# Kernel optimization log

Hardware: AMD Instinct MI355X
Metric: run time of the kernel (lower is better)

Reference implementation:

```python
import jax, jax.numpy as jnp
import numpy as np

NUM_NODES = 100000
NUM_EDGES = 1600000
DIM = 64
NUM_LAYERS = 3


def setup_inputs() -> dict:
    key = jax.random.key(0)
    k1, k2 = jax.random.split(key)
    x = jax.random.normal(k1, (NUM_NODES, DIM), dtype=jnp.float32)
    adj_t = jax.random.randint(k2, (2, NUM_EDGES), 0, NUM_NODES, dtype=jnp.int64)
    return {"x": x, "adj_t": adj_t}


def reference(x, adj_t):
    n = x.shape[0]
    # undirected -> add reversed edges (adj_t_is_undirected=True path)
    edge_index = jnp.concatenate([adj_t, adj_t[::-1]], axis=1)  # [2, 2E]
    row, col = edge_index[0], edge_index[1]
    edge_weight = jnp.ones((row.shape[0],), dtype=x.dtype)
    # gcn_norm: D^-0.5 A D^-0.5 (degree computed by scatter over col)
    deg = jax.ops.segment_sum(edge_weight, col, num_segments=n)
    deg_inv_sqrt = jnp.where(deg > 0, jax.lax.rsqrt(deg), 0.0).astype(x.dtype)
    w = deg_inv_sqrt[row] * edge_weight * deg_inv_sqrt[col]  # [2E]
    outs = [x]
    for _ in range(NUM_LAYERS):
        # gather -> scale -> scatter_add (SpMM)
        msgs = w[:, None] * x[row]                     # [2E, D]
        x = jax.ops.segment_sum(msgs, col, num_segments=n)  # [N, D]
        outs.append(x)
    return jnp.mean(jnp.stack(outs), axis=0)
```

## Files before the change

### kernel.cpp

```cpp
#include <hip/hip_runtime.h>

#define DIM 64
#define BKT_SHIFT 7
#define BKT_G 128
#define NBLK 256
#define HIST_B 1024
#define NREP 4
#define CAP 4608
#define RCAP 18

__device__ inline float blo(unsigned p) { return __uint_as_float(p << 16); }
__device__ inline float bhi(unsigned p) { return __uint_as_float(p & 0xffff0000u); }
__device__ inline unsigned bpack(float x, float y) {
    unsigned ux = __float_as_uint(x);
    unsigned uy = __float_as_uint(y);
    ux += 0x7fffu + ((ux >> 16) & 1u);
    uy += 0x7fffu + ((uy >> 16) & 1u);
    return (ux >> 16) | (uy & 0xffff0000u);
}

__global__ void zero_kernel(int* __restrict__ p, int n) {
    int i = blockIdx.x * blockDim.x + threadIdx.x;
    if (i < n) p[i] = 0;
}

__global__ __launch_bounds__(HIST_B)
void place_direct_kernel(const int* __restrict__ adj, int E,
                         int* __restrict__ gcnt,
                         unsigned* __restrict__ pairs, int NB) {
    extern __shared__ int lds[];
    int* lh  = lds;
    int* cur = lds + NREP * NB;
    for (int g = threadIdx.x; g < (NREP + 1) * NB; g += blockDim.x) lds[g] = 0;
    __syncthreads();
    const int rep = (threadIdx.x & (NREP - 1)) * NB;
    const int n4 = E >> 2;
    const int4* srcs = (const int4*)adj;
    const int4* dsts = (const int4*)(adj + E);

    int4 a0 = {0,0,0,0}, b0 = a0, a1 = a0, b1 = a0;
    int have = 0;
    for (int i = blockIdx.x * blockDim.x + threadIdx.x; i < n4;
         i += NBLK * blockDim.x) {
        int4 a = srcs[i];
        int4 b = dsts[i];
        atomicAdd(&lh[rep + (a.x >> BKT_SHIFT)], 1);
        atomicAdd(&lh[rep + (a.y >> BKT_SHIFT)], 1);
        atomicAdd(&lh[rep + (a.z >> BKT_SHIFT)], 1);
        atomicAdd(&lh[rep + (a.w >> BKT_SHIFT)], 1);
        atomicAdd(&lh[rep + (b.x >> BKT_SHIFT)], 1);
        atomicAdd(&lh[rep + (b.y >> BKT_SHIFT)], 1);
        atomicAdd(&lh[rep + (b.z >> BKT_SHIFT)], 1);
        atomicAdd(&lh[rep + (b.w >> BKT_SHIFT)], 1);
        if (have == 0)      { a0 = a; b0 = b; have = 1; }
        else if (have == 1) { a1 = a; b1 = b; have = 2; }
    }
    int te = 0, ta = 0, tb = 0;
    if (blockIdx.x == 0) {
        for (int e = (n4 << 2) + threadIdx.x; e < E; e += blockDim.x) {
            int a = adj[e];
            int b = adj[E + e];
            atomicAdd(&lh[rep + (a >> BKT_SHIFT)], 1);
            atomicAdd(&lh[rep + (b >> BKT_SHIFT)], 1);
            if (te == 0) { ta = a; tb = b; te = 1; }
        }
    }
    __syncthreads();
    for (int g = threadIdx.x; g < NB; g += blockDim.x) {
        int tot = lh[g] + lh[NB + g] + lh[2 * NB + g] + lh[3 * NB + g];
        cur[g] = (tot > 0) ? atomicAdd(&gcnt[g], tot) : 0;
    }
    __syncthreads();
#define PLACE_EMIT(av, bv)                                                     \
    {                                                                          \
        int gb = (bv) >> BKT_SHIFT;                                            \
        int p = atomicAdd(&cur[gb], 1);                                        \
        if (p < CAP)                                                           \
            pairs[(size_t)gb * CAP + p] =                                      \
                ((unsigned)((bv) & (BKT_G - 1)) << 17) | (unsigned)(av);       \
        int ga = (av) >> BKT_SHIFT;                                            \
        p = atomicAdd(&cur[ga], 1);                                            \
        if (p < CAP)                                                           \
            pairs[(size_t)ga * CAP + p] =                                      \
                ((unsigned)((av) & (BKT_G - 1)) << 17) | (unsigned)(bv);       \
    }
    if (have >= 1) {
        PLACE_EMIT(a0.x, b0.x); PLACE_EMIT(a0.y, b0.y);
        PLACE_EMIT(a0.z, b0.z); PLACE_EMIT(a0.w, b0.w);
    }
    if (have >= 2) {
        PLACE_EMIT(a1.x, b1.x); PLACE_EMIT(a1.y, b1.y);
        PLACE_EMIT(a1.z, b1.z); PLACE_EMIT(a1.w, b1.w);
    }
    {
        int it = 0;
        for (int i = blockIdx.x * blockDim.x + threadIdx.x; i < n4;
             i += NBLK * blockDim.x) {
            if (it >= 2) {
                int4 a = srcs[i];
                int4 b = dsts[i];
                PLACE_EMIT(a.x, b.x); PLACE_EMIT(a.y, b.y);
                PLACE_EMIT(a.z, b.z); PLACE_EMIT(a.w, b.w);
            }
            ++it;
        }
    }
    if (blockIdx.x == 0) {
        int tl = 0;
        for (int e = (n4 << 2) + threadIdx.x; e < E; e += blockDim.x) {
            if (tl == 0 && te == 1) {
                PLACE_EMIT(ta, tb);
            } else {
                int a = adj[e];
                int b = adj[E + e];
                PLACE_EMIT(a, b);
            }
            ++tl;
        }
    }
#undef PLACE_EMIT
}

__global__ void scan782_kernel(const int* __restrict__ gcnt,
                               int* __restrict__ bsums, int nb) {
    __shared__ int tmp[1024];
    int v = (threadIdx.x < nb) ? gcnt[threadIdx.x] : 0;
    tmp[threadIdx.x] = v;
    __syncthreads();
    for (int off = 1; off < 1024; off <<= 1) {
        int t = (threadIdx.x >= off) ? tmp[threadIdx.x - off] : 0;
        __syncthreads();
        tmp[threadIdx.x] += t;
        __syncthreads();
    }
    if (threadIdx.x < nb) bsums[threadIdx.x] = tmp[threadIdx.x] - v;
}

__global__ __launch_bounds__(256)
void pass2_build_kernel(const unsigned* __restrict__ pairs,
                        const int* __restrict__ gcnt,
                        const int* __restrict__ bsums,
                        const float4* __restrict__ x,
                        int* __restrict__ csr_src,
                        int* __restrict__ row_ptr,
                        int* __restrict__ deg,
                        float* __restrict__ dinv,
                        uint4* __restrict__ xs0,
                        int N, int NB, int total_adj) {
    __shared__ int cnt[BKT_G];
    __shared__ int pre[BKT_G];
    __shared__ int cur[BKT_G];
    __shared__ float dv[BKT_G];
    int g = blockIdx.x;
    int base = g << BKT_SHIFT;
    size_t poff = (size_t)g * CAP;
    int m = gcnt[g];
    if (m > CAP) m = CAP;
    int coff = bsums[g];
    if (threadIdx.x < BKT_G) cnt[threadIdx.x] = 0;
    __syncthreads();
    unsigned rec[RCAP];
#pragma unroll
    for (int k = 0; k < RCAP; ++k) {
        int i = threadIdx.x + k * 256;
        unsigned p = 0;
        if (i < m) {
            p = pairs[poff + i];
            atomicAdd(&cnt[p >> 17], 1);
        }
        rec[k] = p;
    }
    __syncthreads();
    if (threadIdx.x < BKT_G) pre[threadIdx.x] = cnt[threadIdx.x];
    __syncthreads();
    for (int o = 1; o < BKT_G; o <<= 1) {
        int t = 0;
        if (threadIdx.x < BKT_G && threadIdx.x >= o) t = pre[threadIdx.x - o];
        __syncthreads();
        if (threadIdx.x < BKT_G) pre[threadIdx.x] += t;
        __syncthreads();
    }
    if (threadIdx.x < BKT_G) {
        int v = base + threadIdx.x;
        if (v < N) {
            int c = cnt[threadIdx.x];
            int start = coff + pre[threadIdx.x] - c;
            float di = (c > 0) ? rsqrtf((float)c) : 0.0f;
            row_ptr[v] = start;
            deg[v] = c;
            dinv[v] = di;
            dv[threadIdx.x] = di;
            cur[threadIdx.x] = start;
        }
    }
    if (g == NB - 1 && threadIdx.x == 0) row_ptr[N] = total_adj;
    __syncthreads();
#pragma unroll
    for (int k = 0; k < RCAP; ++k) {
        int i = threadIdx.x + k * 256;
        if (i < m) {
            unsigned p = rec[k];
            int pos = atomicAdd(&cur[p >> 17], 1);
            csr_src[pos] = (int)(p & 0x1ffffu);
        }
    }
    for (int w = threadIdx.x; w < BKT_G * 8; w += blockDim.x) {
        int vl = w >> 3, sub = w & 7;
        int v = base + vl;
        if (v < N) {
            float di = dv[vl];
            float4 xa = x[(size_t)v * 16 + sub * 2];
            float4 xb = x[(size_t)v * 16 + sub * 2 + 1];
            uint4 o;
            o.x = bpack(di * xa.x, di * xa.y);
            o.y = bpack(di * xa.z, di * xa.w);
            o.z = bpack(di * xb.x, di * xb.y);
            o.w = bpack(di * xb.z, di * xb.w);
            xs0[(size_t)v * 8 + sub] = o;
        }
    }
}

#define SPMM_ACCUM_BODY                                                        \
    int half = threadIdx.x & 31;                                               \
    int nb = half >> 3, sub = half & 7;                                        \
    int beg = row_ptr[v];                                                      \
    int end = row_ptr[v + 1];                                                  \
    int full = (end - beg) >> 4;                                               \
    float a0 = 0, a1 = 0, a2 = 0, a3 = 0, a4 = 0, a5 = 0, a6 = 0, a7 = 0;      \
    int j = beg;                                                               \
    int s0 = 0, s1 = 0, s2 = 0, s3 = 0;                                        \
    if (full > 0) {                                                            \
        int b = j + 4 * nb;                                                    \
        s0 = csr_src[b];     s1 = csr_src[b + 1];                              \
        s2 = csr_src[b + 2]; s3 = csr_src[b + 3];                              \
    }                                                                          \
    for (int it = 0; it < full; ++it) {                                        \
        int jn = j + 16;                                                       \
        int t0 = 0, t1 = 0, t2 = 0, t3 = 0;                                    \
        if (it + 1 < full) {                                                   \
            int b = jn + 4 * nb;                                               \
            t0 = csr_src[b];     t1 = csr_src[b + 1];                          \
            t2 = csr_src[b + 2]; t3 = csr_src[b + 3];                          \
        }                                                                      \
        uint4 p0 = xs_in[(size_t)s0 * 8 + sub];                                \
        uint4 p1 = xs_in[(size_t)s1 * 8 + sub];                                \
        uint4 p2 = xs_in[(size_t)s2 * 8 + sub];                                \
        uint4 p3 = xs_in[(size_t)s3 * 8 + sub];                                \
        a0 += (blo(p0.x) + blo(p1.x)) + (blo(p2.x) + blo(p3.x));               \
        a1 += (bhi(p0.x) + bhi(p1.x)) + (bhi(p2.x) + bhi(p3.x));               \
        a2 += (blo(p0.y) + blo(p1.y)) + (blo(p2.y) + blo(p3.y));               \
        a3 += (bhi(p0.y) + bhi(p1.y)) + (bhi(p2.y) + bhi(p3.y));               \
        a4 += (blo(p0.z) + blo(p1.z)) + (blo(p2.z) + blo(p3.z));               \
        a5 += (bhi(p0.z) + bhi(p1.z)) + (bhi(p2.z) + bhi(p3.z));               \
        a6 += (blo(p0.w) + blo(p1.w)) + (blo(p2.w) + blo(p3.w));               \
        a7 += (bhi(p0.w) + bhi(p1.w)) + (bhi(p2.w) + bhi(p3.w));               \
        s0 = t0; s1 = t1; s2 = t2; s3 = t3;                                    \
        j = jn;                                                                \
    }                                                                          \
    for (int idx = j + nb; idx < end; idx += 4) {                              \
        int s = csr_src[idx];                                                  \
        uint4 p = xs_in[(size_t)s * 8 + sub];                                  \
        a0 += blo(p.x); a1 += bhi(p.x);                                        \
        a2 += blo(p.y); a3 += bhi(p.y);                                        \
        a4 += blo(p.z); a5 += bhi(p.z);                                        \
        a6 += blo(p.w); a7 += bhi(p.w);                                        \
    }                                                                          \
    a0 += __shfl_xor(a0, 8);  a0 += __shfl_xor(a0, 16);                        \
    a1 += __shfl_xor(a1, 8);  a1 += __shfl_xor(a1, 16);                        \
    a2 += __shfl_xor(a2, 8);  a2 += __shfl_xor(a2, 16);                        \
    a3 += __shfl_xor(a3, 8);  a3 += __shfl_xor(a3, 16);                        \
    a4 += __shfl_xor(a4, 8);  a4 += __shfl_xor(a4, 16);                        \
    a5 += __shfl_xor(a5, 8);  a5 += __shfl_xor(a5, 16);                        \
    a6 += __shfl_xor(a6, 8);  a6 += __shfl_xor(a6, 16);                        \
    a7 += __shfl_xor(a7, 8);  a7 += __shfl_xor(a7, 16);

__global__ void spmm_bf16_kernel(const int* __restrict__ row_ptr,
                                 const int* __restrict__ csr_src,
                                 const float* __restrict__ dinv,
                                 const uint4* __restrict__ xs_in,
                                 uint4* __restrict__ xs_out, int N) {
    int t = blockIdx.x * blockDim.x + threadIdx.x;
    int v = t >> 5;
    if (v >= N) return;
    SPMM_ACCUM_BODY
    if (nb == 0) {
        float di = dinv[v];
        float d2 = di * di;
        uint4 o;
        o.x = bpack(d2 * a0, d2 * a1);
        o.y = bpack(d2 * a2, d2 * a3);
        o.z = bpack(d2 * a4, d2 * a5);
        o.w = bpack(d2 * a6, d2 * a7);
        xs_out[(size_t)v * 8 + sub] = o;
    }
}

__global__ void spmm_last_kernel(const int* __restrict__ row_ptr,
                                 const int* __restrict__ csr_src,
                                 const float* __restrict__ dinv,
                                 const int* __restrict__ deg,
                                 const uint4* __restrict__ xs_in,
                                 const uint4* __restrict__ xs1,
                                 const float4* __restrict__ x,
                                 float4* __restrict__ out, int N) {
    int t = blockIdx.x * blockDim.x + threadIdx.x;
    int v = t >> 5;
    if (v >= N) return;
    SPMM_ACCUM_BODY
    if (nb == 0) {
        float di = dinv[v];
        float rs = sqrtf((float)deg[v]);
        size_t idx = (size_t)v * 8 + sub;
        uint4 q1 = xs1[idx];
        uint4 q2 = xs_in[idx];
        float4 xa = x[(size_t)v * 16 + sub * 2];
        float4 xb = x[(size_t)v * 16 + sub * 2 + 1];
        float4 oa, ob;
        oa.x = 0.25f * (xa.x + rs * (blo(q1.x) + blo(q2.x)) + di * a0);
        oa.y = 0.25f * (xa.y + rs * (bhi(q1.x) + bhi(q2.x)) + di * a1);
        oa.z = 0.25f * (xa.z + rs * (blo(q1.y) + blo(q2.y)) + di * a2);
        oa.w = 0.25f * (xa.w + rs * (bhi(q1.y) + bhi(q2.y)) + di * a3);
        ob.x = 0.25f * (xb.x + rs * (blo(q1.z) + blo(q2.z)) + di * a4);
        ob.y = 0.25f * (xb.y + rs * (bhi(q1.z) + bhi(q2.z)) + di * a5);
        ob.z = 0.25f * (xb.z + rs * (blo(q1.w) + blo(q2.w)) + di * a6);
        ob.w = 0.25f * (xb.w + rs * (bhi(q1.w) + bhi(q2.w)) + di * a7);
        out[(size_t)v * 16 + sub * 2]     = oa;
        out[(size_t)v * 16 + sub * 2 + 1] = ob;
    }
}

extern "C" void kernel_launch(void* const* d_in, const int* in_sizes, int n_in,
                              void* d_out, int out_size, void* d_ws, size_t ws_size,
                              hipStream_t stream) {
    const float* x = (const float*)d_in[0];
    const int* adj = (const int*)d_in[1];
    float* out     = (float*)d_out;

    const int total_adj = in_sizes[1];
    const int E = total_adj / 2;
    const int N = in_sizes[0] / DIM;
    const int NB = (N + BKT_G - 1) / BKT_G;

    size_t BUF = (size_t)total_adj * 4;
    size_t xsb = (size_t)N * 32 * 4;
    if (xsb > BUF) BUF = xsb;
    BUF = (BUF + 255) & ~(size_t)255;
    size_t PAIRS_B = ((size_t)NB * CAP * 4 + 255) & ~(size_t)255;

    char* ws = (char*)d_ws;
    int*      deg     = (int*)(ws);
    float*    dinv    = (float*)(ws + (size_t)512 * 1024);
    int*      row_ptr = (int*)(ws + (size_t)1024 * 1024);
    int*      gcnt    = (int*)(ws + (size_t)1536 * 1024);
    int*      bsums   = (int*)(ws + (size_t)1568 * 1024);
    char*     big     = ws + (size_t)1664 * 1024;
    int*      csr_src = (int*)(big);
    unsigned* pairs   = (unsigned*)(big + BUF);
    uint4*    xs0     = (uint4*)(big + BUF + PAIRS_B);
    uint4*    xs1     = (uint4*)(big + BUF + PAIRS_B + BUF);
    uint4*    xs2     = (uint4*)(big + BUF + PAIRS_B + 2 * BUF);

    const int B = 256;

    zero_kernel<<<(NB + 1023) / 1024, 1024, 0, stream>>>(gcnt, NB);

    place_direct_kernel<<<NBLK, HIST_B, (NREP + 1) * NB * sizeof(int), stream>>>(
        adj, E, gcnt, pairs, NB);

    scan782_kernel<<<1, 1024, 0, stream>>>(gcnt, bsums, NB);

    pass2_build_kernel<<<NB, B, 0, stream>>>(pairs, gcnt, bsums, (const float4*)x,
                                             csr_src, row_ptr, deg, dinv,
                                             xs0, N, NB, total_adj);

    const int nblocks32 = (int)(((long long)N * 32 + B - 1) / B);
    spmm_bf16_kernel<<<nblocks32, B, 0, stream>>>(row_ptr, csr_src, dinv, xs0, xs1, N);
    spmm_bf16_kernel<<<nblocks32, B, 0, stream>>>(row_ptr, csr_src, dinv, xs1, xs2, N);
    spmm_last_kernel<<<nblocks32, B, 0, stream>>>(row_ptr, csr_src, dinv, deg,
                                                  xs2, xs1, (const float4*)x,
                                                  (float4*)out, N);
}
```

Before: 288.6 us.

## Fuse bucket prefix scan into build kernel and stage CSR writes in LDS

Drops the single-block scan kernel. Each build block now computes its own global offset by summing the bucket counts of all earlier buckets and reducing them in shared memory. The block also writes its sorted source indices into an LDS window first, then copies them out to csr_src with coalesced writes instead of scattered global stores. The cost is redundant reads of the count array (up to ~782 ints per block) and 18KB of extra LDS per block, which may lower occupancy.

```diff
diff --git a/kernel.cpp b/kernel.cpp
--- a/kernel.cpp
+++ b/kernel.cpp
@@ -121,25 +121,9 @@
 #undef PLACE_EMIT
 }
 
-__global__ void scan782_kernel(const int* __restrict__ gcnt,
-                               int* __restrict__ bsums, int nb) {
-    __shared__ int tmp[1024];
-    int v = (threadIdx.x < nb) ? gcnt[threadIdx.x] : 0;
-    tmp[threadIdx.x] = v;
-    __syncthreads();
-    for (int off = 1; off < 1024; off <<= 1) {
-        int t = (threadIdx.x >= off) ? tmp[threadIdx.x - off] : 0;
-        __syncthreads();
-        tmp[threadIdx.x] += t;
-        __syncthreads();
-    }
-    if (threadIdx.x < nb) bsums[threadIdx.x] = tmp[threadIdx.x] - v;
-}
-
 __global__ __launch_bounds__(256)
 void pass2_build_kernel(const unsigned* __restrict__ pairs,
                         const int* __restrict__ gcnt,
-                        const int* __restrict__ bsums,
                         const float4* __restrict__ x,
                         int* __restrict__ csr_src,
                         int* __restrict__ row_ptr,
@@ -151,14 +135,23 @@
     __shared__ int pre[BKT_G];
     __shared__ int cur[BKT_G];
     __shared__ float dv[BKT_G];
+    __shared__ int win[CAP];
+    __shared__ int red[256];
     int g = blockIdx.x;
     int base = g << BKT_SHIFT;
     size_t poff = (size_t)g * CAP;
     int m = gcnt[g];
     if (m > CAP) m = CAP;
-    int coff = bsums[g];
+    int lsum = 0;
+    for (int h = threadIdx.x; h < g; h += 256) lsum += gcnt[h];
+    red[threadIdx.x] = lsum;
     if (threadIdx.x < BKT_G) cnt[threadIdx.x] = 0;
     __syncthreads();
+    for (int o = 128; o > 0; o >>= 1) {
+        if (threadIdx.x < o) red[threadIdx.x] += red[threadIdx.x + o];
+        __syncthreads();
+    }
+    int coff = red[0];
     unsigned rec[RCAP];
 #pragma unroll
     for (int k = 0; k < RCAP; ++k) {
@@ -184,13 +177,13 @@
         int v = base + threadIdx.x;
         if (v < N) {
             int c = cnt[threadIdx.x];
-            int start = coff + pre[threadIdx.x] - c;
+            int lstart = pre[threadIdx.x] - c;
             float di = (c > 0) ? rsqrtf((float)c) : 0.0f;
-            row_ptr[v] = start;
+            row_ptr[v] = coff + lstart;
             deg[v] = c;
             dinv[v] = di;
             dv[threadIdx.x] = di;
-            cur[threadIdx.x] = start;
+            cur[threadIdx.x] = lstart;
         }
     }
     if (g == NB - 1 && threadIdx.x == 0) row_ptr[N] = total_adj;
@@ -201,9 +194,12 @@
         if (i < m) {
             unsigned p = rec[k];
             int pos = atomicAdd(&cur[p >> 17], 1);
-            csr_src[pos] = (int)(p & 0x1ffffu);
-        }
-    }
+            win[pos] = (int)(p & 0x1ffffu);
+        }
+    }
+    __syncthreads();
+    for (int i = threadIdx.x; i < m; i += 256)
+        csr_src[coff + i] = win[i];
     for (int w = threadIdx.x; w < BKT_G * 8; w += blockDim.x) {
         int vl = w >> 3, sub = w & 7;
         int v = base + vl;
@@ -353,7 +349,6 @@
     float*    dinv    = (float*)(ws + (size_t)512 * 1024);
     int*      row_ptr = (int*)(ws + (size_t)1024 * 1024);
     int*      gcnt    = (int*)(ws + (size_t)1536 * 1024);
-    int*      bsums   = (int*)(ws + (size_t)1568 * 1024);
     char*     big     = ws + (size_t)1664 * 1024;
     int*      csr_src = (int*)(big);
     unsigned* pairs   = (unsigned*)(big + BUF);
@@ -368,9 +363,7 @@
     place_direct_kernel<<<NBLK, HIST_B, (NREP + 1) * NB * sizeof(int), stream>>>(
         adj, E, gcnt, pairs, NB);
 
-    scan782_kernel<<<1, 1024, 0, stream>>>(gcnt, bsums, NB);
-
-    pass2_build_kernel<<<NB, B, 0, stream>>>(pairs, gcnt, bsums, (const float4*)x,
+    pass2_build_kernel<<<NB, B, 0, stream>>>(pairs, gcnt, (const float4*)x,
                                              csr_src, row_ptr, deg, dinv,
                                              xs0, N, NB, total_adj);
 
```

Result: faster. 279.7 us (-3.1%).
